# Kernel optimization log

Hardware: AMD Instinct MI355X
Metric: run time of the kernel (lower is better)

Reference implementation:

```python
import jax, jax.numpy as jnp
import numpy as np

N = 50000      # nodes
E = 800000     # directed edges (avg degree 16 in/out pairs)
F_IN = 16      # dataset.num_features
H = 64         # neuron
S = 7          # Chebyshev order


def setup_inputs() -> dict:
    key = jax.random.key(0)
    ks = jax.random.split(key, 12)
    x = jax.random.normal(ks[0], (N, F_IN), dtype=jnp.float32)
    row = jax.random.randint(ks[1], (E,), 0, N, dtype=jnp.int32)
    off = jax.random.randint(ks[2], (E,), 1, N, dtype=jnp.int32)
    col = (row + off) % N  # guarantees no self-loops (PyG removes them)
    edge_index = jnp.stack([row, col])
    lambda_max = jnp.array([2.0], dtype=jnp.float32)
    def lin(k, fi, fo):
        return jax.random.normal(k, (S, fi, fo), dtype=jnp.float32) * (1.0 / np.sqrt(fi))
    W1 = lin(ks[3], F_IN, H); b1 = jnp.zeros((H,), jnp.float32)
    W2 = lin(ks[4], H, H);    b2 = jnp.zeros((H,), jnp.float32)
    W3 = lin(ks[5], H, H);    b3 = jnp.zeros((H,), jnp.float32)
    Wfc = jax.random.normal(ks[6], (H, 1), dtype=jnp.float32) * (1.0 / np.sqrt(H))
    bfc = jnp.zeros((1,), jnp.float32)
    return {"x": x, "edge_index": edge_index, "lambda_max": lambda_max,
            "W1": W1, "b1": b1, "W2": W2, "b2": b2, "W3": W3, "b3": b3,
            "Wfc": Wfc, "bfc": bfc}


def _make_spmv(edge_index, lam, n):
    # L_hat = 2/lambda_max * (I - D^-1/2 A D^-1/2) - I  (PyG ChebConv sym norm)
    row, col = edge_index[0], edge_index[1]
    deg = jax.ops.segment_sum(jnp.ones_like(row, dtype=jnp.float32), row, num_segments=n)
    dis = jnp.where(deg > 0, jax.lax.rsqrt(jnp.maximum(deg, 1.0)), 0.0)
    w = -(2.0 / lam) * dis[row] * dis[col]      # off-diagonal edge weights
    diag = 2.0 / lam - 1.0                       # self-loop weight
    def spmv(xx):  # L_hat @ xx
        return jax.ops.segment_sum(w[:, None] * xx[col], row, num_segments=n) + diag * xx
    return spmv


def _cheb(xx, W, b, spmv):
    Tx0 = xx
    out = Tx0 @ W[0]
    Tx1 = spmv(Tx0)
    out = out + Tx1 @ W[1]
    for k in range(2, W.shape[0]):  # fixed small S loop
        Tx2 = 2.0 * spmv(Tx1) - Tx0
        out = out + Tx2 @ W[k]
        Tx0, Tx1 = Tx1, Tx2
    return out + b


def reference(x, edge_index, lambda_max, W1, b1, W2, b2, W3, b3, Wfc, bfc):
    lam = lambda_max[0]
    spmv = _make_spmv(edge_index, lam, x.shape[0])
    h = jax.nn.relu(_cheb(x, W1, b1, spmv))
    h = jax.nn.relu(_cheb(h, W2, b2, spmv))
    h = jax.nn.relu(_cheb(h, W3, b3, spmv))
    return h @ Wfc + bfc
```

## Files before the change

kernel.cpp:

```cpp
#include <hip/hip_runtime.h>
#include <math.h>


#define WS_ALIGN(x) (((size_t)(x) + 255) & ~(size_t)255)

using f16x8 = __attribute__((ext_vector_type(8))) _Float16;
using f32x4 = __attribute__((ext_vector_type(4))) float;

__device__ inline float h2f_bits(unsigned int b) {
  unsigned short s = (unsigned short)(b & 0xffffu);
  _Float16 h;
  __builtin_memcpy(&h, &s, 2);
  return (float)h;
}
__device__ inline unsigned short f2h_bits(float f) {
  _Float16 h = (_Float16)f;
  unsigned short s;
  __builtin_memcpy(&s, &h, 2);
  return s;
}
union H8 {
  uint4 q;
  _Float16 h[8];
  ushort us[8];
};

__global__ __launch_bounds__(256) void hist_kernel(const int* __restrict__ row, int E,
                                                   int* __restrict__ deg) {
  int i = blockIdx.x * 256 + threadIdx.x;
  if (i < E) atomicAdd(&deg[row[i]], 1);
}

__global__ __launch_bounds__(256) void scan_sum_kernel(const int* __restrict__ deg,
                                                       int* __restrict__ bsum, int n) {
  int base = blockIdx.x * 1024 + threadIdx.x;
  int v = 0;
#pragma unroll
  for (int u = 0; u < 4; ++u) {
    int i = base + u * 256;
    if (i < n) v += deg[i];
  }
#pragma unroll
  for (int off = 32; off > 0; off >>= 1) v += __shfl_down(v, off, 64);
  __shared__ int ws[4];
  int lane = threadIdx.x & 63, wave = threadIdx.x >> 6;
  if (lane == 0) ws[wave] = v;
  __syncthreads();
  if (threadIdx.x == 0) bsum[blockIdx.x] = ws[0] + ws[1] + ws[2] + ws[3];
}

__global__ __launch_bounds__(64) void scan_bsum_kernel(int* __restrict__ bsum, int nb) {
  int t = threadIdx.x;
  int v = (t < nb) ? bsum[t] : 0;
  int sc = v;
#pragma unroll
  for (int off = 1; off < 64; off <<= 1) {
    int tv = __shfl_up(sc, off, 64);
    if (t >= off) sc += tv;
  }
  if (t < nb) bsum[t] = sc - v;
}

__global__ __launch_bounds__(256) void scan_out_kernel(const int* __restrict__ deg,
                                                       const int* __restrict__ bsum,
                                                       int* __restrict__ row_ptr,
                                                       int* __restrict__ cursor,
                                                       float* __restrict__ dis, int n) {
  int base = blockIdx.x * 1024 + threadIdx.x * 4;
  int loc[4];
  int s = 0;
#pragma unroll
  for (int u = 0; u < 4; ++u) {
    int i = base + u;
    loc[u] = (i < n) ? deg[i] : 0;
    s += loc[u];
  }
  int lane = threadIdx.x & 63, wave = threadIdx.x >> 6;
  int sc = s;
#pragma unroll
  for (int off = 1; off < 64; off <<= 1) {
    int tv = __shfl_up(sc, off, 64);
    if (lane >= off) sc += tv;
  }
  __shared__ int wtot[4];
  if (lane == 63) wtot[wave] = sc;
  __syncthreads();
  int pre = sc - s + bsum[blockIdx.x];
  for (int w = 0; w < wave; ++w) pre += wtot[w];
  if (blockIdx.x == 0 && threadIdx.x == 0) row_ptr[0] = 0;
  int running = pre;
#pragma unroll
  for (int u = 0; u < 4; ++u) {
    int i = base + u;
    if (i < n) {
      cursor[i] = running;
      dis[i] = (loc[u] > 0) ? (1.0f / sqrtf((float)loc[u])) : 0.0f;
      running += loc[u];
      row_ptr[i + 1] = running;
    }
  }
}

__global__ __launch_bounds__(256) void scatter_x8(const int* __restrict__ row,
                                                  const int* __restrict__ col, int E,
                                                  int* __restrict__ cursor,
                                                  const float* __restrict__ dis,
                                                  const float* __restrict__ lamp,
                                                  unsigned int* __restrict__ cw, int n) {
  int c = blockIdx.x & 7;
  int j = blockIdx.x >> 3;
  int nj = gridDim.x >> 3;
  int lo = (c * n) >> 3;
  int hi = ((c + 1) * n) >> 3;
  float sc = -(2.0f / lamp[0]);
  for (int i = j * 256 + threadIdx.x; i < E; i += nj * 256) {
    int r = row[i];
    if (r < lo || r >= hi) continue;
    int cc = col[i];
    int pos = atomicAdd(&cursor[r], 1);
    float w = sc * dis[r] * dis[cc];
    cw[pos] = ((unsigned int)cc << 16) | (unsigned int)f2h_bits(w);
  }
}

__device__ inline void wpk_pack(const float* __restrict__ W, ushort* __restrict__ Wpk,
                                int KREAL, int t) {
  int kt = t >> 8, nt = (t >> 6) & 3, l = t & 63;
  int col = nt * 16 + (l & 15);
  int kb = kt * 32 + ((l >> 4) << 3);
  ushort tmp[8];
#pragma unroll
  for (int j = 0; j < 8; ++j) {
    int k = kb + j;
    float v = (k < KREAL) ? W[(size_t)k * 64 + col] : 0.0f;
    tmp[j] = f2h_bits(v);
  }
  ushort4* dst = (ushort4*)Wpk + (size_t)((kt * 4 + nt) * 64 + l) * 2;
  dst[0] = make_ushort4(tmp[0], tmp[1], tmp[2], tmp[3]);
  dst[1] = make_ushort4(tmp[4], tmp[5], tmp[6], tmp[7]);
}

__global__ __launch_bounds__(256) void prep_all_kernel(
    const float* __restrict__ W1, const float* __restrict__ W2,
    const float* __restrict__ W3, ushort* __restrict__ Wpk1, ushort* __restrict__ Wpk2,
    ushort* __restrict__ Wpk3, const float* __restrict__ x, ushort* __restrict__ T1,
    int n) {
  int b = blockIdx.x;
  if (b < 4) {
    wpk_pack(W1, Wpk1, 112, b * 256 + threadIdx.x);
  } else if (b < 18) {
    wpk_pack(W2, Wpk2, 448, (b - 4) * 256 + threadIdx.x);
  } else if (b < 32) {
    wpk_pack(W3, Wpk3, 448, (b - 18) * 256 + threadIdx.x);
  } else {
    int t = (b - 32) * 256 + threadIdx.x;
    if (t < n * 4) {
      int row = t >> 2, q = t & 3;
      float4 v = ((const float4*)x)[(size_t)row * 4 + q];
      ushort4 o;
      o.x = f2h_bits(v.x);
      o.y = f2h_bits(v.y);
      o.z = f2h_bits(v.z);
      o.w = f2h_bits(v.w);
      ((ushort4*)T1)[(size_t)row * 4 + q] = o;
    } else if (t < n * 8) {
      int t2 = t - n * 4;
      ((ushort4*)(T1 + (size_t)7 * n * 16))[t2] = make_ushort4(0, 0, 0, 0);
    }
  }
}

template <int SW, int MODE, int SLICES>
__global__ __launch_bounds__(256) void spmv_slice(const int* __restrict__ row_ptr,
                                                  const unsigned int* __restrict__ cw,
                                                  const float* __restrict__ lamp,
                                                  const ushort* __restrict__ xin,
                                                  const ushort* __restrict__ sub,
                                                  ushort* __restrict__ xout, int ssz,
                                                  int n) {
  constexpr int LPR = SW / 8;
  constexpr int RPB = 256 / LPR;
  constexpr int B = 16;
  constexpr int EPL = B / LPR;
  int bx = blockIdx.x;
  if (SLICES == 2) {
    int sl = bx & 1;
    bx >>= 1;
    xin += (size_t)sl * ssz;
    if (MODE == 1) sub += (size_t)sl * ssz;
    xout += (size_t)sl * ssz;
  }
  int i = bx * RPB + threadIdx.y;
  if (i >= n) return;
  int f8 = threadIdx.x;
  int lane = (threadIdx.y * LPR + f8) & 63;
  int grpbase = lane - f8;
  float diag = 2.0f / lamp[0] - 1.0f;
  H8 xd;
  xd.q = *(const uint4*)(xin + (size_t)i * SW + f8 * 8);
  float a[8];
#pragma unroll
  for (int j = 0; j < 8; ++j) a[j] = diag * (float)xd.h[j];
  int s = row_ptr[i], e = row_ptr[i + 1];

  for (int j0 = s; j0 < e; j0 += B) {
    unsigned int pv[EPL];
#pragma unroll
    for (int u = 0; u < EPL; ++u) {
      int jj = j0 + f8 * EPL + u;
      pv[u] = cw[jj < e ? jj : (e - 1)];
    }
    H8 xv[B];
    float ww[B];
#pragma unroll
    for (int u = 0; u < B; ++u) {
      unsigned int pu = (unsigned int)__shfl((int)pv[u % EPL], grpbase + u / EPL, 64);
      bool valid = (j0 + u) < e;
      ww[u] = valid ? h2f_bits(pu) : 0.0f;
      int ad = valid ? (int)(pu >> 16) : i;
      xv[u].q = *(const uint4*)(xin + (size_t)ad * SW + f8 * 8);
    }
#pragma unroll
    for (int u = 0; u < B; ++u)
#pragma unroll
      for (int j = 0; j < 8; ++j) a[j] += ww[u] * (float)xv[u].h[j];
  }

  float r[8];
  if (MODE == 1) {
    H8 sv;
    sv.q = *(const uint4*)(sub + (size_t)i * SW + f8 * 8);
#pragma unroll
    for (int j = 0; j < 8; ++j) r[j] = 2.0f * a[j] - (float)sv.h[j];
  } else {
#pragma unroll
    for (int j = 0; j < 8; ++j) r[j] = a[j];
  }
  H8 o;
#pragma unroll
  for (int j = 0; j < 8; ++j) o.us[j] = f2h_bits(r[j]);
  *(uint4*)(xout + (size_t)i * SW + f8 * 8) = o.q;
}

template <int SW, int KT, bool LAST>
__global__ __launch_bounds__(256) void gemm_mfma(const ushort* __restrict__ A,
                                                 const ushort* __restrict__ Wpk,
                                                 const float* __restrict__ bias,
                                                 ushort* __restrict__ dsth,
                                                 const float* __restrict__ wfc,
                                                 const float* __restrict__ bfc,
                                                 float* __restrict__ dout, int n) {
  int l = threadIdx.x & 63;
  int tile = blockIdx.x * 4 + (threadIdx.x >> 6);
  int r0 = tile * 16;
  if (r0 >= n) return;
  size_t slotsz = (size_t)n * SW;
  int row = r0 + (l & 15);
  const f16x8* bp = (const f16x8*)Wpk + l;
  f32x4 c[4] = {{0.f, 0.f, 0.f, 0.f},
                {0.f, 0.f, 0.f, 0.f},
                {0.f, 0.f, 0.f, 0.f},
                {0.f, 0.f, 0.f, 0.f}};
#pragma unroll
  for (int kt = 0; kt < KT; ++kt) {
    int slot, off;
    if constexpr (SW == 32) {
      slot = kt;
      off = (l >> 4) << 3;
    } else {
      slot = 2 * kt + ((l >> 4) >> 1);
      off = ((l >> 4) & 1) << 3;
    }
    f16x8 af = *(const f16x8*)(A + slot * slotsz + (size_t)row * SW + off);
#pragma unroll
    for (int nt = 0; nt < 4; ++nt) {
      f16x8 bf = bp[(kt * 4 + nt) * 64];
      c[nt] = __builtin_amdgcn_mfma_f32_16x16x32_f16(af, bf, c[nt], 0, 0, 0);
    }
  }
  int rb = r0 + ((l >> 4) << 2);
  int cc = l & 15;
  if (LAST) {
    float bfc0 = bfc[0];
#pragma unroll
    for (int j = 0; j < 4; ++j) {
      float part = 0.0f;
#pragma unroll
      for (int nt = 0; nt < 4; ++nt) {
        int col = nt * 16 + cc;
        part += fmaxf(c[nt][j] + bias[col], 0.0f) * wfc[col];
      }
#pragma unroll
      for (int m = 1; m < 16; m <<= 1) part += __shfl_xor(part, m, 64);
      if (cc == 0) dout[rb + j] = part + bfc0;
    }
  } else {
    size_t dslot = (size_t)n * 32;
#pragma unroll
    for (int nt = 0; nt < 4; ++nt) {
      int col = nt * 16 + cc;
      float bv = bias[col];
      ushort* dbase = dsth + (col >> 5) * dslot + (col & 31);
#pragma unroll
      for (int j = 0; j < 4; ++j) {
        float v = fmaxf(c[nt][j] + bv, 0.0f);
        dbase[(size_t)(rb + j) * 32] = f2h_bits(v);
      }
    }
  }
}

extern "C" void kernel_launch(void* const* d_in, const int* in_sizes, int n_in, void* d_out,
                              int out_size, void* d_ws, size_t ws_size, hipStream_t stream) {
  const float* x = (const float*)d_in[0];
  const int* ei = (const int*)d_in[1];
  const float* lamp = (const float*)d_in[2];
  const float* W1 = (const float*)d_in[3];
  const float* b1 = (const float*)d_in[4];
  const float* W2 = (const float*)d_in[5];
  const float* b2 = (const float*)d_in[6];
  const float* W3 = (const float*)d_in[7];
  const float* b3 = (const float*)d_in[8];
  const float* Wfc = (const float*)d_in[9];
  const float* bfc = (const float*)d_in[10];

  const int N = in_sizes[0] / 16;
  const int E = in_sizes[1] / 2;
  const int* row = ei;
  const int* col = ei + E;

  char* p = (char*)d_ws;
  auto alloc = [&](size_t bytes) {
    char* r = p;
    p += WS_ALIGN(bytes);
    return r;
  };
  int* deg = (int*)alloc((size_t)N * 4);
  int* row_ptr = (int*)alloc((size_t)(N + 1) * 4);
  int* cursor = (int*)alloc((size_t)N * 4);
  unsigned int* cw = (unsigned int*)alloc((size_t)E * 4);
  float* dis = (float*)alloc((size_t)N * 4);
  int* bsum = (int*)alloc(256 * 4);
  ushort* T1 = (ushort*)alloc((size_t)8 * N * 16 * 2);
  ushort* TXC = (ushort*)alloc((size_t)14 * N * 32 * 2);
  ushort* Wpk1 = (ushort*)alloc((size_t)4 * 256 * 8 * 2);
  ushort* Wpk2 = (ushort*)alloc((size_t)14 * 256 * 8 * 2);
  ushort* Wpk3 = (ushort*)alloc((size_t)14 * 256 * 8 * 2);
  (void)ws_size;
  (void)n_in;
  (void)out_size;

  (void)hipMemsetAsync(deg, 0, (size_t)N * 4, stream);
  hist_kernel<<<(E + 255) / 256, 256, 0, stream>>>(row, E, deg);
  int nb = (N + 1023) / 1024;
  scan_sum_kernel<<<nb, 256, 0, stream>>>(deg, bsum, N);
  scan_bsum_kernel<<<1, 64, 0, stream>>>(bsum, nb);
  scan_out_kernel<<<nb, 256, 0, stream>>>(deg, bsum, row_ptr, cursor, dis, N);
  scatter_x8<<<2048, 256, 0, stream>>>(row, col, E, cursor, dis, lamp, cw, N);

  prep_all_kernel<<<32 + (N * 8 + 255) / 256, 256, 0, stream>>>(W1, W2, W3, Wpk1, Wpk2, Wpk3,
                                                                x, T1, N);

  {
    int ssz = N * 16;
    auto S = [&](int k) { return T1 + (size_t)k * ssz; };
    dim3 bs(2, 128);
    int gs = (N + 127) / 128;
    spmv_slice<16, 0, 1><<<gs, bs, 0, stream>>>(row_ptr, cw, lamp, S(0), nullptr, S(1), ssz,
                                                N);
    for (int k = 2; k < 7; ++k)
      spmv_slice<16, 1, 1><<<gs, bs, 0, stream>>>(row_ptr, cw, lamp, S(k - 1), S(k - 2), S(k),
                                                  ssz, N);
    gemm_mfma<16, 4, false><<<(N / 16 + 3) / 4 + 1, 256, 0, stream>>>(T1, Wpk1, b1, TXC,
                                                                      nullptr, nullptr,
                                                                      nullptr, N);
  }

  for (int layer = 2; layer <= 3; ++layer) {
    int ssz = N * 32;
    auto S = [&](int k) { return TXC + (size_t)(2 * k) * ssz; };
    dim3 bs(4, 64);
    int gs = 2 * ((N + 63) / 64);
    spmv_slice<32, 0, 2><<<gs, bs, 0, stream>>>(row_ptr, cw, lamp, S(0), nullptr, S(1), ssz,
                                                N);
    for (int k = 2; k < 7; ++k)
      spmv_slice<32, 1, 2><<<gs, bs, 0, stream>>>(row_ptr, cw, lamp, S(k - 1), S(k - 2), S(k),
                                                  ssz, N);
    if (layer == 2)
      gemm_mfma<32, 14, false><<<(N / 16 + 3) / 4 + 1, 256, 0, stream>>>(TXC, Wpk2, b2, TXC,
                                                                         nullptr, nullptr,
                                                                         nullptr, N);
    else
      gemm_mfma<32, 14, true><<<(N / 16 + 3) / 4 + 1, 256, 0, stream>>>(TXC, Wpk3, b3,
                                                                        nullptr, Wfc, bfc,
                                                                        (float*)d_out, N);
  }
}
```

Measured before the change: 418.4 us.

## Process SpMV rows in degree-sorted order and halve edge batch size

Adds a counting sort of nodes by degree (histogram, scan, place kernels) to build a permutation, and SpMV blocks process rows through that permutation so rows in a wavefront have similar degree, reducing loop-trip divergence. The edge batch per iteration drops from 16 to 8 so degree-16 rows waste fewer padded lanes. This costs three extra small kernels and an indirection per row, and output writes become scattered rather than contiguous.

Result: slower. 440.6 us (+5.3%).

```diff
diff --git a/kernel.cpp b/kernel.cpp
--- a/kernel.cpp
+++ b/kernel.cpp
@@ -120,6 +120,56 @@
     int pos = atomicAdd(&cursor[r], 1);
     float w = sc * dis[r] * dis[cc];
     cw[pos] = ((unsigned int)cc << 16) | (unsigned int)f2h_bits(w);
+  }
+}
+
+__global__ __launch_bounds__(256) void binc_kernel(const int* __restrict__ deg,
+                                                   int* __restrict__ cnt, int n) {
+  __shared__ int h[64];
+  if (threadIdx.x < 64) h[threadIdx.x] = 0;
+  __syncthreads();
+  int base = blockIdx.x * 1024 + threadIdx.x * 4;
+#pragma unroll
+  for (int u = 0; u < 4; ++u) {
+    int i = base + u;
+    if (i < n) atomicAdd(&h[min(deg[i], 63)], 1);
+  }
+  __syncthreads();
+  if (threadIdx.x < 64) cnt[blockIdx.x * 64 + threadIdx.x] = h[threadIdx.x];
+}
+
+__global__ __launch_bounds__(64) void binscan_kernel(int* __restrict__ cnt, int nbk) {
+  int b = threadIdx.x;
+  int run = 0;
+  for (int k = 0; k < nbk; ++k) {
+    int c = cnt[k * 64 + b];
+    cnt[k * 64 + b] = run;
+    run += c;
+  }
+  int sc = run;
+#pragma unroll
+  for (int off = 1; off < 64; off <<= 1) {
+    int tv = __shfl_up(sc, off, 64);
+    if (b >= off) sc += tv;
+  }
+  int base = sc - run;
+  for (int k = 0; k < nbk; ++k) cnt[k * 64 + b] += base;
+}
+
+__global__ __launch_bounds__(256) void binplace_kernel(const int* __restrict__ deg,
+                                                       const int* __restrict__ cnt,
+                                                       int* __restrict__ perm, int n) {
+  __shared__ int cur[64];
+  if (threadIdx.x < 64) cur[threadIdx.x] = cnt[blockIdx.x * 64 + threadIdx.x];
+  __syncthreads();
+  int base = blockIdx.x * 1024 + threadIdx.x * 4;
+#pragma unroll
+  for (int u = 0; u < 4; ++u) {
+    int i = base + u;
+    if (i < n) {
+      int p = atomicAdd(&cur[min(deg[i], 63)], 1);
+      perm[p] = i;
+    }
   }
 }
 
@@ -174,13 +224,14 @@
 __global__ __launch_bounds__(256) void spmv_slice(const int* __restrict__ row_ptr,
                                                   const unsigned int* __restrict__ cw,
                                                   const float* __restrict__ lamp,
+                                                  const int* __restrict__ perm,
                                                   const ushort* __restrict__ xin,
                                                   const ushort* __restrict__ sub,
                                                   ushort* __restrict__ xout, int ssz,
                                                   int n) {
   constexpr int LPR = SW / 8;
   constexpr int RPB = 256 / LPR;
-  constexpr int B = 16;
+  constexpr int B = 8;
   constexpr int EPL = B / LPR;
   int bx = blockIdx.x;
   if (SLICES == 2) {
@@ -190,8 +241,9 @@
     if (MODE == 1) sub += (size_t)sl * ssz;
     xout += (size_t)sl * ssz;
   }
-  int i = bx * RPB + threadIdx.y;
-  if (i >= n) return;
+  int slot = bx * RPB + threadIdx.y;
+  if (slot >= n) return;
+  int i = perm[slot];
   int f8 = threadIdx.x;
   int lane = (threadIdx.y * LPR + f8) & 63;
   int grpbase = lane - f8;
@@ -341,6 +393,8 @@
   unsigned int* cw = (unsigned int*)alloc((size_t)E * 4);
   float* dis = (float*)alloc((size_t)N * 4);
   int* bsum = (int*)alloc(256 * 4);
+  int* perm = (int*)alloc((size_t)N * 4);
+  int* cnt = (int*)alloc((size_t)((N + 1023) / 1024) * 64 * 4);
   ushort* T1 = (ushort*)alloc((size_t)8 * N * 16 * 2);
   ushort* TXC = (ushort*)alloc((size_t)14 * N * 32 * 2);
   ushort* Wpk1 = (ushort*)alloc((size_t)4 * 256 * 8 * 2);
@@ -358,6 +412,10 @@
   scan_out_kernel<<<nb, 256, 0, stream>>>(deg, bsum, row_ptr, cursor, dis, N);
   scatter_x8<<<2048, 256, 0, stream>>>(row, col, E, cursor, dis, lamp, cw, N);
 
+  binc_kernel<<<nb, 256, 0, stream>>>(deg, cnt, N);
+  binscan_kernel<<<1, 64, 0, stream>>>(cnt, nb);
+  binplace_kernel<<<nb, 256, 0, stream>>>(deg, cnt, perm, N);
+
   prep_all_kernel<<<32 + (N * 8 + 255) / 256, 256, 0, stream>>>(W1, W2, W3, Wpk1, Wpk2, Wpk3,
                                                                 x, T1, N);
 
@@ -366,11 +424,11 @@
     auto S = [&](int k) { return T1 + (size_t)k * ssz; };
     dim3 bs(2, 128);
     int gs = (N + 127) / 128;
-    spmv_slice<16, 0, 1><<<gs, bs, 0, stream>>>(row_ptr, cw, lamp, S(0), nullptr, S(1), ssz,
-                                                N);
+    spmv_slice<16, 0, 1><<<gs, bs, 0, stream>>>(row_ptr, cw, lamp, perm, S(0), nullptr, S(1),
+                                                ssz, N);
     for (int k = 2; k < 7; ++k)
-      spmv_slice<16, 1, 1><<<gs, bs, 0, stream>>>(row_ptr, cw, lamp, S(k - 1), S(k - 2), S(k),
-                                                  ssz, N);
+      spmv_slice<16, 1, 1><<<gs, bs, 0, stream>>>(row_ptr, cw, lamp, perm, S(k - 1), S(k - 2),
+                                                  S(k), ssz, N);
     gemm_mfma<16, 4, false><<<(N / 16 + 3) / 4 + 1, 256, 0, stream>>>(T1, Wpk1, b1, TXC,
                                                                       nullptr, nullptr,
                                                                       nullptr, N);
@@ -381,11 +439,11 @@
     auto S = [&](int k) { return TXC + (size_t)(2 * k) * ssz; };
     dim3 bs(4, 64);
     int gs = 2 * ((N + 63) / 64);
-    spmv_slice<32, 0, 2><<<gs, bs, 0, stream>>>(row_ptr, cw, lamp, S(0), nullptr, S(1), ssz,
-                                                N);
+    spmv_slice<32, 0, 2><<<gs, bs, 0, stream>>>(row_ptr, cw, lamp, perm, S(0), nullptr, S(1),
+                                                ssz, N);
     for (int k = 2; k < 7; ++k)
-      spmv_slice<32, 1, 2><<<gs, bs, 0, stream>>>(row_ptr, cw, lamp, S(k - 1), S(k - 2), S(k),
-                                                  ssz, N);
+      spmv_slice<32, 1, 2><<<gs, bs, 0, stream>>>(row_ptr, cw, lamp, perm, S(k - 1), S(k - 2),
+                                                  S(k), ssz, N);
     if (layer == 2)
       gemm_mfma<32, 14, false><<<(N / 16 + 3) / 4 + 1, 256, 0, stream>>>(TXC, Wpk2, b2, TXC,
                                                                          nullptr, nullptr,
```
